# Optimization experiments

Measured on AMD Instinct MI355X. Metric: run time of the kernel, lower is better.

Reference implementation:

```python
import jax, jax.numpy as jnp
import numpy as np

HIDDEN = 4096
NUM_HEADS = 32
NUM_KV_HEADS = 8
HEAD_DIM = HIDDEN // NUM_HEADS  # 128
ROPE_THETA = 10000.0
T = 2048


def setup_inputs() -> dict:
    key = jax.random.key(0)
    k1, k2, k3 = jax.random.split(key, 3)
    positions = jnp.arange(T, dtype=jnp.int32)
    hidden_states = jax.random.normal(k1, (T, HIDDEN), dtype=jnp.float32)
    # 0.02 init scale keeps logits in a sane range
    Wqkv = jax.random.normal(k2, (HIDDEN, (NUM_HEADS + 2 * NUM_KV_HEADS) * HEAD_DIM), dtype=jnp.float32) * 0.02
    Wo = jax.random.normal(k3, (HIDDEN, HIDDEN), dtype=jnp.float32) * 0.02
    return {"positions": positions, "hidden_states": hidden_states, "Wqkv": Wqkv, "Wo": Wo}


def _rope_neox(x, positions):
    # x: [T, H, D]; neox style rotates halves of the head dim
    d2 = HEAD_DIM // 2
    inv_freq = ROPE_THETA ** (-jnp.arange(0, d2, dtype=jnp.float32) / d2)
    ang = positions.astype(jnp.float32)[:, None] * inv_freq  # [T, d2]
    cos = jnp.cos(ang)[:, None, :]  # [T,1,d2]
    sin = jnp.sin(ang)[:, None, :]
    x1, x2 = x[..., :d2], x[..., d2:]
    return jnp.concatenate([x1 * cos - x2 * sin, x2 * cos + x1 * sin], axis=-1)


def reference(positions, hidden_states, Wqkv, Wo):
    Tn = hidden_states.shape[0]
    q_sz = NUM_HEADS * HEAD_DIM
    kv_sz = NUM_KV_HEADS * HEAD_DIM
    qkv = hidden_states @ Wqkv  # [T, q_sz + 2*kv_sz]
    q = qkv[:, :q_sz].reshape(Tn, NUM_HEADS, HEAD_DIM)
    k = qkv[:, q_sz:q_sz + kv_sz].reshape(Tn, NUM_KV_HEADS, HEAD_DIM)
    v = qkv[:, q_sz + kv_sz:].reshape(Tn, NUM_KV_HEADS, HEAD_DIM)
    q = _rope_neox(q, positions)
    k = _rope_neox(k, positions)
    # GQA: repeat kv heads to match q heads
    rep = NUM_HEADS // NUM_KV_HEADS
    k = jnp.repeat(k, rep, axis=1)  # [T, H, D]
    v = jnp.repeat(v, rep, axis=1)
    scale = HEAD_DIM ** -0.5
    scores = jnp.einsum('thd,shd->hts', q, k) * scale  # [H, T, T]
    causal = positions[:, None] >= positions[None, :]  # [T, T]
    scores = jnp.where(causal[None, :, :], scores, jnp.float32(-1e30))
    probs = jax.nn.softmax(scores, axis=-1)
    attn = jnp.einsum('hts,shd->thd', probs, v).reshape(Tn, HIDDEN)
    return attn @ Wo
```

## Files before the change

### kernel.cpp

```cpp
#include <hip/hip_runtime.h>
#include <hip/hip_bf16.h>
#include <math.h>

#define T_SEQ 2048
#define HID   4096
#define NH    32
#define NKV   8
#define HD    128
#define QKVD  6144
#define KOFF  4096
#define VOFF  5120

typedef unsigned short u16;
typedef unsigned int   u32;
typedef __attribute__((ext_vector_type(4))) float f32x4;
typedef __attribute__((ext_vector_type(8))) short s16x8;
typedef __attribute__((ext_vector_type(4))) unsigned short u16x4;

__device__ inline u16 f2bf(float f) {
  u32 u = __float_as_uint(f);
  u32 r = u + 0x7FFFu + ((u >> 16) & 1u);
  return (u16)(r >> 16);
}
__device__ inline float bf2f(u16 h) { return __uint_as_float(((u32)h) << 16); }

__device__ inline void gl_lds16(const void* g, void* l) {
  __builtin_amdgcn_global_load_lds((const __attribute__((address_space(1))) void*)g,
                                   (__attribute__((address_space(3))) void*)l, 16, 0, 0);
}

__global__ void cast_f32_bf16(const float* __restrict__ in, u16* __restrict__ out, int n) {
  int i = (blockIdx.x * blockDim.x + threadIdx.x) * 4;
  if (i < n) {
    float4 v = *(const float4*)(in + i);
    u16x4 o = { f2bf(v.x), f2bf(v.y), f2bf(v.z), f2bf(v.w) };
    *(u16x4*)(out + i) = o;
  }
}

__global__ void transpose_cast(const float* __restrict__ in, u16* __restrict__ out, int K, int N) {
  __shared__ float tile[32][33];
  int n0 = blockIdx.x * 32, k0 = blockIdx.y * 32;
  int tx = threadIdx.x, ty = threadIdx.y;
  for (int i = ty; i < 32; i += 8)
    tile[i][tx] = in[(size_t)(k0 + i) * N + n0 + tx];
  __syncthreads();
  for (int i = ty; i < 32; i += 8)
    out[(size_t)(n0 + i) * K + k0 + tx] = f2bf(tile[tx][i]);
}

__global__ void vtrans(const u16* __restrict__ qkv, u16* __restrict__ Vt) {
  __shared__ u16 tile[32][33];
  int kv = blockIdx.z;
  int t0 = blockIdx.x * 32, d0 = blockIdx.y * 32;
  int tx = threadIdx.x, ty = threadIdx.y;
  for (int i = ty; i < 32; i += 8)
    tile[i][tx] = qkv[(size_t)(t0 + i) * QKVD + VOFF + kv * HD + d0 + tx];
  __syncthreads();
  for (int i = ty; i < 32; i += 8)
    Vt[(size_t)(kv * HD + d0 + i) * T_SEQ + t0 + tx] = tile[tx][i];
}

__global__ void rope_kernel(u16* __restrict__ qkv, const int* __restrict__ positions) {
  int t = blockIdx.x;
  int h = blockIdx.y * 4 + (threadIdx.x >> 6);
  int i = threadIdx.x & 63;
  float pos = (float)positions[t];
  float freq = exp2f(-(float)i * (13.287712379549449f / 64.0f));
  float ang = pos * freq;
  float s, c;
  sincosf(ang, &s, &c);
  size_t off;
  if (h < NH) off = (size_t)t * QKVD + h * HD;
  else        off = (size_t)t * QKVD + KOFF + (h - NH) * HD;
  float x1 = bf2f(qkv[off + i]);
  float x2 = bf2f(qkv[off + 64 + i]);
  qkv[off + i]      = f2bf(x1 * c - x2 * s);
  qkv[off + 64 + i] = f2bf(x2 * c + x1 * s);
}

__device__ inline void stage_half(const u16* __restrict__ G, int K, u16* lds, int w, int l) {
  const int rl = l >> 3;
  const int cs = ((l & 7) ^ rl) << 3;
#pragma unroll
  for (int i = 0; i < 2; i++) {
    const u16* src = G + (size_t)(8 * w + 64 * i + rl) * K + cs;
    gl_lds16(src, lds + (8 * w + 64 * i) * 64);
  }
}

#define LDA(i, kk) a[i][kk] = *(const s16x8*)(Ah + (((i) * 16 + lr) * 64) + ((((kk) * 4 + lg) ^ xsw) << 3))
#define LDB(j, kk) b[j][kk] = *(const s16x8*)(Bh + (((j) * 16 + lr) * 64) + ((((kk) * 4 + lg) ^ xsw) << 3))
#define MFMA_Q(i0, j0)                                                        \
  _Pragma("unroll") for (int i = 0; i < 4; i++)                               \
  _Pragma("unroll") for (int j = 0; j < 2; j++)                               \
  _Pragma("unroll") for (int kk = 0; kk < 2; kk++)                            \
    acc[i0 + i][j0 + j] = __builtin_amdgcn_mfma_f32_16x16x32_bf16(            \
        a[i0 + i][kk], b[j0 + j][kk], acc[i0 + i][j0 + j], 0, 0, 0);

template <bool BF16OUT>
__global__ __launch_bounds__(512, 2) void gemm256(const u16* __restrict__ A,
                                                  const u16* __restrict__ B,
                                                  void* __restrict__ Cv,
                                                  int M, int N, int K) {
  __shared__ __align__(16) u16 As[2][2][128 * 64];
  __shared__ __align__(16) u16 Bs[2][2][128 * 64];
  const int tid = threadIdx.x;
  const int w = tid >> 6, l = tid & 63;
  const int lr = l & 15, lg = l >> 4;
  const int wm = w >> 2, wn = w & 3;
  const int xsw = lr & 7;
  const int bm = blockIdx.y * 256, bn = blockIdx.x * 256;
  const int NT = K >> 6;

  const u16* Ab0 = A + (size_t)bm * K;
  const u16* Ab1 = A + (size_t)(bm + 128) * K;
  const u16* Bb0 = B + (size_t)bn * K;
  const u16* Bb1 = B + (size_t)(bn + 128) * K;

  f32x4 acc[8][4] = {};

  stage_half(Ab0, K, As[0][0], w, l);
  stage_half(Ab1, K, As[0][1], w, l);
  stage_half(Bb0, K, Bs[0][0], w, l);
  stage_half(Bb1, K, Bs[0][1], w, l);
  if (NT > 1) {
    stage_half(Ab0 + 64, K, As[1][0], w, l);
    stage_half(Ab1 + 64, K, As[1][1], w, l);
    asm volatile("s_waitcnt vmcnt(4)" ::: "memory");
  } else {
    asm volatile("s_waitcnt vmcnt(0)" ::: "memory");
  }
  __builtin_amdgcn_s_barrier();

  for (int t = 0; t < NT; t++) {
    const int cur = t & 1;
    const u16* Ah = &As[cur][wm][0];
    const u16* Bh = &Bs[cur][wn >> 1][(wn & 1) * 64 * 64];
    s16x8 a[8][2], b[4][2];

#pragma unroll
    for (int i = 0; i < 4; i++) { LDA(i, 0); LDA(i, 1); }
    LDB(0, 0); LDB(0, 1); LDB(1, 0); LDB(1, 1);
    if (t + 1 < NT) stage_half(Bb0 + (size_t)(t + 1) * 64, K, Bs[cur ^ 1][0], w, l);
    __builtin_amdgcn_s_barrier();
    asm volatile("s_waitcnt lgkmcnt(0)" ::: "memory");
    __builtin_amdgcn_s_setprio(1);
    MFMA_Q(0, 0)
    __builtin_amdgcn_s_setprio(0);
    __builtin_amdgcn_s_barrier();

#pragma unroll
    for (int i = 4; i < 8; i++) { LDA(i, 0); LDA(i, 1); }
    LDB(2, 0); LDB(2, 1); LDB(3, 0); LDB(3, 1);
    if (t + 1 < NT) stage_half(Bb1 + (size_t)(t + 1) * 64, K, Bs[cur ^ 1][1], w, l);
    __builtin_amdgcn_s_barrier();
    asm volatile("s_waitcnt lgkmcnt(0)" ::: "memory");
    __builtin_amdgcn_s_setprio(1);
    MFMA_Q(0, 2)
    __builtin_amdgcn_s_setprio(0);
    __builtin_amdgcn_s_barrier();

    if (t + 2 < NT) stage_half(Ab0 + (size_t)(t + 2) * 64, K, As[cur][0], w, l);
    __builtin_amdgcn_s_barrier();
    __builtin_amdgcn_s_setprio(1);
    MFMA_Q(4, 2)
    __builtin_amdgcn_s_setprio(0);
    __builtin_amdgcn_s_barrier();

    if (t + 2 < NT) {
      stage_half(Ab1 + (size_t)(t + 2) * 64, K, As[cur][1], w, l);
      asm volatile("s_waitcnt vmcnt(4)" ::: "memory");
    } else {
      asm volatile("s_waitcnt vmcnt(0)" ::: "memory");
    }
    __builtin_amdgcn_s_barrier();
    __builtin_amdgcn_s_setprio(1);
    MFMA_Q(4, 0)
    __builtin_amdgcn_s_setprio(0);
    __builtin_amdgcn_s_barrier();
  }

#pragma unroll
  for (int i = 0; i < 8; i++)
#pragma unroll
    for (int j = 0; j < 4; j++)
#pragma unroll
      for (int r = 0; r < 4; r++) {
        int row = bm + wm * 128 + i * 16 + lg * 4 + r;
        int col = bn + wn * 64 + j * 16 + lr;
        float v = acc[i][j][r];
        if (BF16OUT) ((u16*)Cv)[(size_t)row * N + col] = f2bf(v);
        else         ((float*)Cv)[(size_t)row * N + col] = v;
      }
}
#undef LDA
#undef LDB
#undef MFMA_Q

__device__ inline void stage_tiles(const u16* __restrict__ qkv, const u16* __restrict__ Vt,
                                   u16* Kb, u16* Vb, int kv0, int hkv, int w, int l) {
  const int krow_l = l >> 4;
  const int kcb = (l & 15) << 4;
  const int vrow_l = l >> 3;
  const int vcb = (l & 7) << 4;
#pragma unroll
  for (int c = 0; c < 4; c++) {
    int row = c * 16 + w * 4 + krow_l;
    const char* src = (const char*)(qkv + (size_t)(kv0 + row) * QKVD + KOFF + hkv * HD) +
                      (kcb ^ ((row & 7) << 4));
    gl_lds16(src, (char*)Kb + (c * 16 + w * 4) * 256);
  }
#pragma unroll
  for (int c = 0; c < 4; c++) {
    int row = c * 32 + w * 8 + vrow_l;
    const char* src = (const char*)(Vt + (size_t)(hkv * HD + row) * T_SEQ + kv0) +
                      (vcb ^ ((row & 7) << 4));
    gl_lds16(src, (char*)Vb + (c * 32 + w * 8) * 128);
  }
}

__global__ __launch_bounds__(256) void attn_fwd(const u16* __restrict__ qkv, const u16* __restrict__ Vt,
                                                u16* __restrict__ attnout) {
  __shared__ __align__(16) u16 Ks[2][64 * 128];
  __shared__ __align__(16) u16 Vs[2][128 * 64];
  __shared__ __align__(16) u16 plds[4][16 * 72];
  const int tid = threadIdx.x;
  const int w = tid >> 6, l = tid & 63;
  const int lr = l & 15, g = l >> 4;
  const int h = blockIdx.y;
  const int hkv = h >> 2;
  const int swzl = (lr & 7) << 4;
  const float scale = 0.08838834764831845f;
  u16* pw = &plds[w][0];

  for (int seg = 0; seg < 2; seg++) {
    const int qt = (seg == 0) ? blockIdx.x : (31 - blockIdx.x);
    const int q0 = qt * 64 + w * 16;
    const int q_abs = q0 + lr;

    s16x8 qf[4];
    const u16* qbase = qkv + (size_t)(q0 + lr) * QKVD + h * HD + g * 8;
#pragma unroll
    for (int kk = 0; kk < 4; kk++) qf[kk] = *(const s16x8*)(qbase + kk * 32);

    f32x4 acc_o[8] = {};
    float m_run = -__builtin_inff();
    float l_run = 0.0f;
    const int nt = qt + 1;

    stage_tiles(qkv, Vt, Ks[0], Vs[0], 0, hkv, w, l);
    asm volatile("s_waitcnt vmcnt(0)" ::: "memory");
    __syncthreads();
    int cur = 0;
    for (int kt = 0; kt < nt; kt++) {
      const int kv0 = kt * 64;
      if (kt + 1 < nt)
        stage_tiles(qkv, Vt, Ks[cur ^ 1], Vs[cur ^ 1], kv0 + 64, hkv, w, l);
      const bool masked = (kt == qt);

      f32x4 sa[4];
      const char* kb = (const char*)Ks[cur];
#pragma unroll
      for (int ct = 0; ct < 4; ct++) {
        f32x4 aa = {0.f, 0.f, 0.f, 0.f};
#pragma unroll
        for (int kk = 0; kk < 4; kk++) {
          s16x8 kf = *(const s16x8*)(kb + (ct * 16 + lr) * 256 + (((kk << 6) + (g << 4)) ^ swzl));
          aa = __builtin_amdgcn_mfma_f32_16x16x32_bf16(kf, qf[kk], aa, 0, 0, 0);
        }
        sa[ct] = aa;
      }

      float p[16];
      float pmax = -__builtin_inff();
#pragma unroll
      for (int ct = 0; ct < 4; ct++)
#pragma unroll
        for (int r = 0; r < 4; r++) {
          float s = sa[ct][r] * scale;
          if (masked) {
            int kv_abs = kv0 + ct * 16 + g * 4 + r;
            if (kv_abs > q_abs) s = -__builtin_inff();
          }
          p[ct * 4 + r] = s;
          pmax = fmaxf(pmax, s);
        }
      pmax = fmaxf(pmax, __shfl_xor(pmax, 16, 64));
      pmax = fmaxf(pmax, __shfl_xor(pmax, 32, 64));
      float m_new = fmaxf(m_run, pmax);
      float fac = __expf(m_run - m_new);
      float psum = 0.f;
#pragma unroll
      for (int x = 0; x < 16; x++) {
        float e = __expf(p[x] - m_new);
        p[x] = e;
        psum += e;
      }
      psum += __shfl_xor(psum, 16, 64);
      psum += __shfl_xor(psum, 32, 64);
      l_run = l_run * fac + psum;
      m_run = m_new;
      float fr[4];
#pragma unroll
      for (int r = 0; r < 4; r++) fr[r] = __shfl(fac, g * 4 + r, 64);
#pragma unroll
      for (int dt = 0; dt < 8; dt++)
#pragma unroll
        for (int r = 0; r < 4; r++) acc_o[dt][r] *= fr[r];

#pragma unroll
      for (int ct = 0; ct < 4; ct++) {
        u16x4 pk = { f2bf(p[ct * 4 + 0]), f2bf(p[ct * 4 + 1]), f2bf(p[ct * 4 + 2]), f2bf(p[ct * 4 + 3]) };
        *(u16x4*)(pw + lr * 72 + ct * 16 + g * 4) = pk;
      }
      asm volatile("s_waitcnt lgkmcnt(0)" ::: "memory");
      __builtin_amdgcn_sched_barrier(0);
      s16x8 pa0 = *(const s16x8*)(pw + lr * 72 + g * 8);
      s16x8 pa1 = *(const s16x8*)(pw + lr * 72 + 32 + g * 8);

      const char* vbb = (const char*)Vs[cur];
#pragma unroll
      for (int dt = 0; dt < 8; dt++) {
        s16x8 v0 = *(const s16x8*)(vbb + (dt * 16 + lr) * 128 + ((g << 4) ^ swzl));
        s16x8 v1 = *(const s16x8*)(vbb + (dt * 16 + lr) * 128 + ((64 + (g << 4)) ^ swzl));
        acc_o[dt] = __builtin_amdgcn_mfma_f32_16x16x32_bf16(pa0, v0, acc_o[dt], 0, 0, 0);
        acc_o[dt] = __builtin_amdgcn_mfma_f32_16x16x32_bf16(pa1, v1, acc_o[dt], 0, 0, 0);
      }
      asm volatile("s_waitcnt vmcnt(0)" ::: "memory");
      __syncthreads();
      cur ^= 1;
    }

    float ln[4];
#pragma unroll
    for (int r = 0; r < 4; r++) ln[r] = __shfl(l_run, g * 4 + r, 64);
#pragma unroll
    for (int dt = 0; dt < 8; dt++)
#pragma unroll
      for (int r = 0; r < 4; r++) {
        int row = q0 + g * 4 + r;
        int col = h * HD + dt * 16 + lr;
        attnout[(size_t)row * HID + col] = f2bf(acc_o[dt][r] / ln[r]);
      }
  }
}

extern "C" void kernel_launch(void* const* d_in, const int* in_sizes, int n_in,
                              void* d_out, int out_size, void* d_ws, size_t ws_size,
                              hipStream_t stream) {
  const int*   positions = (const int*)d_in[0];
  const float* X         = (const float*)d_in[1];
  const float* Wqkv      = (const float*)d_in[2];
  const float* Wo        = (const float*)d_in[3];
  float* out = (float*)d_out;

  char* ws = (char*)d_ws;
  size_t off = 0;
  u16* Xbf    = (u16*)(ws + off); off += (size_t)T_SEQ * HID * 2;
  u16* Wqkvt  = (u16*)(ws + off); off += (size_t)QKVD * HID * 2;
  u16* Wot    = (u16*)(ws + off); off += (size_t)HID * HID * 2;
  u16* qkv    = (u16*)(ws + off); off += (size_t)T_SEQ * QKVD * 2;
  u16* Vt     = (u16*)(ws + off); off += (size_t)NKV * HD * T_SEQ * 2;
  u16* attnb  = (u16*)(ws + off); off += (size_t)T_SEQ * HID * 2;

  cast_f32_bf16<<<dim3((T_SEQ * HID) / (256 * 4)), dim3(256), 0, stream>>>(X, Xbf, T_SEQ * HID);
  transpose_cast<<<dim3(QKVD / 32, HID / 32), dim3(32, 8), 0, stream>>>(Wqkv, Wqkvt, HID, QKVD);
  transpose_cast<<<dim3(HID / 32, HID / 32), dim3(32, 8), 0, stream>>>(Wo, Wot, HID, HID);
  gemm256<true><<<dim3(QKVD / 256, T_SEQ / 256), dim3(512), 0, stream>>>(Xbf, Wqkvt, qkv, T_SEQ, QKVD, HID);
  rope_kernel<<<dim3(T_SEQ, 10), dim3(256), 0, stream>>>(qkv, positions);
  vtrans<<<dim3(T_SEQ / 32, HD / 32, NKV), dim3(32, 8), 0, stream>>>(qkv, Vt);
  attn_fwd<<<dim3(16, 32), dim3(256), 0, stream>>>(qkv, Vt, attnb);
  gemm256<false><<<dim3(HID / 256, T_SEQ / 256), dim3(512), 0, stream>>>(attnb, Wot, out, T_SEQ, HID, HID);
}
```

Measured before the change: 585.7 us.

## Specialize QKV and output GEMMs with new tile shapes and triple buffering

Replaces the shared 256x256 GEMM with two specialized kernels. The QKV GEMM uses 256x192 tiles, giving 256 blocks instead of 192 to better fill the CUs. The output GEMM uses 128x256 tiles with a three-stage LDS ring buffer, giving 256 blocks and deeper prefetch. The goal is to reduce wave quantization and hide load latency, at the cost of lower per-block arithmetic intensity and more LDS per block.

```diff
diff --git a/kernel.cpp b/kernel.cpp
--- a/kernel.cpp
+++ b/kernel.cpp
@@ -79,104 +79,113 @@
   qkv[off + 64 + i] = f2bf(x2 * c + x1 * s);
 }
 
-__device__ inline void stage_half(const u16* __restrict__ G, int K, u16* lds, int w, int l) {
+__device__ inline void stage_unit(const u16* __restrict__ G, int K, u16* lds, int w, int l) {
   const int rl = l >> 3;
+  const int row = 8 * w + rl;
   const int cs = ((l & 7) ^ rl) << 3;
-#pragma unroll
-  for (int i = 0; i < 2; i++) {
-    const u16* src = G + (size_t)(8 * w + 64 * i + rl) * K + cs;
-    gl_lds16(src, lds + (8 * w + 64 * i) * 64);
-  }
-}
-
-#define LDA(i, kk) a[i][kk] = *(const s16x8*)(Ah + (((i) * 16 + lr) * 64) + ((((kk) * 4 + lg) ^ xsw) << 3))
-#define LDB(j, kk) b[j][kk] = *(const s16x8*)(Bh + (((j) * 16 + lr) * 64) + ((((kk) * 4 + lg) ^ xsw) << 3))
-#define MFMA_Q(i0, j0)                                                        \
-  _Pragma("unroll") for (int i = 0; i < 4; i++)                               \
-  _Pragma("unroll") for (int j = 0; j < 2; j++)                               \
-  _Pragma("unroll") for (int kk = 0; kk < 2; kk++)                            \
-    acc[i0 + i][j0 + j] = __builtin_amdgcn_mfma_f32_16x16x32_bf16(            \
-        a[i0 + i][kk], b[j0 + j][kk], acc[i0 + i][j0 + j], 0, 0, 0);
-
-template <bool BF16OUT>
-__global__ __launch_bounds__(512, 2) void gemm256(const u16* __restrict__ A,
-                                                  const u16* __restrict__ B,
-                                                  void* __restrict__ Cv,
-                                                  int M, int N, int K) {
-  __shared__ __align__(16) u16 As[2][2][128 * 64];
-  __shared__ __align__(16) u16 Bs[2][2][128 * 64];
+  gl_lds16(G + (size_t)row * K + cs, lds + 8 * w * 64);
+}
+
+#define RD(base, row) (*(const s16x8*)((base) + (size_t)(row) * 64 + ((((kk) * 4 + lg) ^ xsw) << 3)))
+#define MM(i, j) acc[i][j] = __builtin_amdgcn_mfma_f32_16x16x32_bf16(a[i][kk], b[j][kk], acc[i][j], 0, 0, 0)
+
+__global__ __launch_bounds__(512, 2) void gemm_qkv(const u16* __restrict__ A, const u16* __restrict__ B,
+                                                   u16* __restrict__ C, int M, int N, int K) {
+  __shared__ __align__(16) u16 As[2][256 * 64];
+  __shared__ __align__(16) u16 Bs[2][192 * 64];
   const int tid = threadIdx.x;
   const int w = tid >> 6, l = tid & 63;
   const int lr = l & 15, lg = l >> 4;
   const int wm = w >> 2, wn = w & 3;
   const int xsw = lr & 7;
-  const int bm = blockIdx.y * 256, bn = blockIdx.x * 256;
+  const int bm = blockIdx.y * 256, bn = blockIdx.x * 192;
   const int NT = K >> 6;
 
-  const u16* Ab0 = A + (size_t)bm * K;
-  const u16* Ab1 = A + (size_t)(bm + 128) * K;
-  const u16* Bb0 = B + (size_t)bn * K;
-  const u16* Bb1 = B + (size_t)(bn + 128) * K;
-
-  f32x4 acc[8][4] = {};
-
-  stage_half(Ab0, K, As[0][0], w, l);
-  stage_half(Ab1, K, As[0][1], w, l);
-  stage_half(Bb0, K, Bs[0][0], w, l);
-  stage_half(Bb1, K, Bs[0][1], w, l);
-  if (NT > 1) {
-    stage_half(Ab0 + 64, K, As[1][0], w, l);
-    stage_half(Ab1 + 64, K, As[1][1], w, l);
-    asm volatile("s_waitcnt vmcnt(4)" ::: "memory");
-  } else {
-    asm volatile("s_waitcnt vmcnt(0)" ::: "memory");
-  }
+  f32x4 acc[8][3] = {};
+  s16x8 a[8][2], b[3][2];
+
+#pragma unroll
+  for (int u = 0; u < 4; u++) stage_unit(A + (size_t)(bm + 64 * u) * K, K, As[0] + u * 4096, w, l);
+#pragma unroll
+  for (int u = 0; u < 3; u++) stage_unit(B + (size_t)(bn + 64 * u) * K, K, Bs[0] + u * 4096, w, l);
+#pragma unroll
+  for (int u = 0; u < 4; u++) stage_unit(A + (size_t)(bm + 64 * u) * K + 64, K, As[1] + u * 4096, w, l);
+  asm volatile("s_waitcnt vmcnt(4)" ::: "memory");
   __builtin_amdgcn_s_barrier();
 
   for (int t = 0; t < NT; t++) {
     const int cur = t & 1;
-    const u16* Ah = &As[cur][wm][0];
-    const u16* Bh = &Bs[cur][wn >> 1][(wn & 1) * 64 * 64];
-    s16x8 a[8][2], b[4][2];
-
-#pragma unroll
-    for (int i = 0; i < 4; i++) { LDA(i, 0); LDA(i, 1); }
-    LDB(0, 0); LDB(0, 1); LDB(1, 0); LDB(1, 1);
-    if (t + 1 < NT) stage_half(Bb0 + (size_t)(t + 1) * 64, K, Bs[cur ^ 1][0], w, l);
+    const u16* Ah = As[cur];
+    const u16* Bh = Bs[cur];
+    const int k1 = (t + 1) * 64, k2 = (t + 2) * 64;
+
+#pragma unroll
+    for (int kk = 0; kk < 2; kk++) {
+#pragma unroll
+      for (int i = 0; i < 4; i++) a[i][kk] = RD(Ah, wm * 128 + i * 16 + lr);
+#pragma unroll
+      for (int j = 0; j < 2; j++) b[j][kk] = RD(Bh, wn * 48 + j * 16 + lr);
+    }
+    if (t + 1 < NT) {
+      stage_unit(B + (size_t)(bn) * K + k1, K, Bs[cur ^ 1] + 0 * 4096, w, l);
+      stage_unit(B + (size_t)(bn + 64) * K + k1, K, Bs[cur ^ 1] + 1 * 4096, w, l);
+    }
     __builtin_amdgcn_s_barrier();
     asm volatile("s_waitcnt lgkmcnt(0)" ::: "memory");
-    __builtin_amdgcn_s_setprio(1);
-    MFMA_Q(0, 0)
-    __builtin_amdgcn_s_setprio(0);
-    __builtin_amdgcn_s_barrier();
-
-#pragma unroll
-    for (int i = 4; i < 8; i++) { LDA(i, 0); LDA(i, 1); }
-    LDB(2, 0); LDB(2, 1); LDB(3, 0); LDB(3, 1);
-    if (t + 1 < NT) stage_half(Bb1 + (size_t)(t + 1) * 64, K, Bs[cur ^ 1][1], w, l);
+    __builtin_amdgcn_sched_barrier(0);
+    __builtin_amdgcn_s_setprio(1);
+#pragma unroll
+    for (int kk = 0; kk < 2; kk++)
+#pragma unroll
+      for (int i = 0; i < 4; i++) { MM(i, 0); MM(i, 1); }
+    __builtin_amdgcn_s_setprio(0);
+    __builtin_amdgcn_s_barrier();
+
+#pragma unroll
+    for (int kk = 0; kk < 2; kk++) {
+#pragma unroll
+      for (int i = 4; i < 8; i++) a[i][kk] = RD(Ah, wm * 128 + i * 16 + lr);
+      b[2][kk] = RD(Bh, wn * 48 + 2 * 16 + lr);
+    }
+    if (t + 1 < NT)
+      stage_unit(B + (size_t)(bn + 128) * K + k1, K, Bs[cur ^ 1] + 2 * 4096, w, l);
     __builtin_amdgcn_s_barrier();
     asm volatile("s_waitcnt lgkmcnt(0)" ::: "memory");
-    __builtin_amdgcn_s_setprio(1);
-    MFMA_Q(0, 2)
-    __builtin_amdgcn_s_setprio(0);
-    __builtin_amdgcn_s_barrier();
-
-    if (t + 2 < NT) stage_half(Ab0 + (size_t)(t + 2) * 64, K, As[cur][0], w, l);
-    __builtin_amdgcn_s_barrier();
-    __builtin_amdgcn_s_setprio(1);
-    MFMA_Q(4, 2)
+    __builtin_amdgcn_sched_barrier(0);
+    __builtin_amdgcn_s_setprio(1);
+#pragma unroll
+    for (int kk = 0; kk < 2; kk++)
+#pragma unroll
+      for (int i = 0; i < 8; i++) MM(i, 2);
     __builtin_amdgcn_s_setprio(0);
     __builtin_amdgcn_s_barrier();
 
     if (t + 2 < NT) {
-      stage_half(Ab1 + (size_t)(t + 2) * 64, K, As[cur][1], w, l);
+      stage_unit(A + (size_t)(bm) * K + k2, K, As[cur] + 0 * 4096, w, l);
+      stage_unit(A + (size_t)(bm + 64) * K + k2, K, As[cur] + 1 * 4096, w, l);
+    }
+    __builtin_amdgcn_s_barrier();
+    __builtin_amdgcn_s_setprio(1);
+#pragma unroll
+    for (int kk = 0; kk < 2; kk++)
+#pragma unroll
+      for (int i = 4; i < 8; i++) MM(i, 0);
+    __builtin_amdgcn_s_setprio(0);
+    __builtin_amdgcn_s_barrier();
+
+    if (t + 2 < NT) {
+      stage_unit(A + (size_t)(bm + 128) * K + k2, K, As[cur] + 2 * 4096, w, l);
+      stage_unit(A + (size_t)(bm + 192) * K + k2, K, As[cur] + 3 * 4096, w, l);
       asm volatile("s_waitcnt vmcnt(4)" ::: "memory");
     } else {
       asm volatile("s_waitcnt vmcnt(0)" ::: "memory");
     }
     __builtin_amdgcn_s_barrier();
     __builtin_amdgcn_s_setprio(1);
-    MFMA_Q(4, 0)
+#pragma unroll
+    for (int kk = 0; kk < 2; kk++)
+#pragma unroll
+      for (int i = 4; i < 8; i++) MM(i, 1);
     __builtin_amdgcn_s_setprio(0);
     __builtin_amdgcn_s_barrier();
   }
@@ -184,19 +193,112 @@
 #pragma unroll
   for (int i = 0; i < 8; i++)
 #pragma unroll
-    for (int j = 0; j < 4; j++)
+    for (int j = 0; j < 3; j++)
 #pragma unroll
       for (int r = 0; r < 4; r++) {
         int row = bm + wm * 128 + i * 16 + lg * 4 + r;
+        int col = bn + wn * 48 + j * 16 + lr;
+        C[(size_t)row * N + col] = f2bf(acc[i][j][r]);
+      }
+}
+
+__global__ __launch_bounds__(512, 2) void gemm_out(const u16* __restrict__ A, const u16* __restrict__ B,
+                                                   float* __restrict__ C, int M, int N, int K) {
+  __shared__ __align__(16) u16 As3[3 * 128 * 64];
+  __shared__ __align__(16) u16 Bs3[3 * 256 * 64];
+  const int tid = threadIdx.x;
+  const int w = tid >> 6, l = tid & 63;
+  const int lr = l & 15, lg = l >> 4;
+  const int wm = w >> 2, wn = w & 3;
+  const int xsw = lr & 7;
+  const int bm = blockIdx.y * 128, bn = blockIdx.x * 256;
+  const int NT = K >> 6;
+
+  f32x4 acc[4][4] = {};
+  s16x8 a[4][2], b[4][2];
+
+#pragma unroll
+  for (int u = 0; u < 2; u++) stage_unit(A + (size_t)(bm + 64 * u) * K, K, As3 + u * 4096, w, l);
+#pragma unroll
+  for (int u = 0; u < 4; u++) stage_unit(B + (size_t)(bn + 64 * u) * K, K, Bs3 + u * 4096, w, l);
+#pragma unroll
+  for (int u = 0; u < 2; u++) stage_unit(A + (size_t)(bm + 64 * u) * K + 64, K, As3 + 8192 + u * 4096, w, l);
+#pragma unroll
+  for (int u = 0; u < 4; u++) stage_unit(B + (size_t)(bn + 64 * u) * K + 64, K, Bs3 + 16384 + u * 4096, w, l);
+  asm volatile("s_waitcnt vmcnt(6)" ::: "memory");
+  __builtin_amdgcn_s_barrier();
+
+  int cur = 0;
+  for (int t = 0; t < NT; t++) {
+    const u16* Ah = As3 + cur * 8192;
+    const u16* Bh = Bs3 + cur * 16384;
+    int sb = cur + 2; if (sb >= 3) sb -= 3;
+    u16* Asb = As3 + sb * 8192;
+    u16* Bsb = Bs3 + sb * 16384;
+    const int k2 = (t + 2) * 64;
+
+#pragma unroll
+    for (int kk = 0; kk < 2; kk++) {
+#pragma unroll
+      for (int i = 0; i < 4; i++) a[i][kk] = RD(Ah, wm * 64 + i * 16 + lr);
+#pragma unroll
+      for (int j = 0; j < 2; j++) b[j][kk] = RD(Bh, wn * 64 + j * 16 + lr);
+    }
+    if (t + 2 < NT) {
+      stage_unit(B + (size_t)(bn) * K + k2, K, Bsb + 0 * 4096, w, l);
+      stage_unit(B + (size_t)(bn + 64) * K + k2, K, Bsb + 1 * 4096, w, l);
+      stage_unit(B + (size_t)(bn + 128) * K + k2, K, Bsb + 2 * 4096, w, l);
+    }
+    __builtin_amdgcn_s_barrier();
+    asm volatile("s_waitcnt lgkmcnt(0)" ::: "memory");
+    __builtin_amdgcn_sched_barrier(0);
+    __builtin_amdgcn_s_setprio(1);
+#pragma unroll
+    for (int kk = 0; kk < 2; kk++)
+#pragma unroll
+      for (int i = 0; i < 4; i++) { MM(i, 0); MM(i, 1); }
+    __builtin_amdgcn_s_setprio(0);
+    __builtin_amdgcn_s_barrier();
+
+#pragma unroll
+    for (int kk = 0; kk < 2; kk++)
+#pragma unroll
+      for (int j = 2; j < 4; j++) b[j][kk] = RD(Bh, wn * 64 + j * 16 + lr);
+    if (t + 2 < NT) {
+      stage_unit(B + (size_t)(bn + 192) * K + k2, K, Bsb + 3 * 4096, w, l);
+      stage_unit(A + (size_t)(bm) * K + k2, K, Asb + 0 * 4096, w, l);
+      stage_unit(A + (size_t)(bm + 64) * K + k2, K, Asb + 1 * 4096, w, l);
+      asm volatile("s_waitcnt vmcnt(6)" ::: "memory");
+    } else {
+      asm volatile("s_waitcnt vmcnt(0)" ::: "memory");
+    }
+    __builtin_amdgcn_s_barrier();
+    asm volatile("s_waitcnt lgkmcnt(0)" ::: "memory");
+    __builtin_amdgcn_sched_barrier(0);
+    __builtin_amdgcn_s_setprio(1);
+#pragma unroll
+    for (int kk = 0; kk < 2; kk++)
+#pragma unroll
+      for (int i = 0; i < 4; i++) { MM(i, 2); MM(i, 3); }
+    __builtin_amdgcn_s_setprio(0);
+    __builtin_amdgcn_s_barrier();
+
+    cur = (cur == 2) ? 0 : cur + 1;
+  }
+
+#pragma unroll
+  for (int i = 0; i < 4; i++)
+#pragma unroll
+    for (int j = 0; j < 4; j++)
+#pragma unroll
+      for (int r = 0; r < 4; r++) {
+        int row = bm + wm * 64 + i * 16 + lg * 4 + r;
         int col = bn + wn * 64 + j * 16 + lr;
-        float v = acc[i][j][r];
-        if (BF16OUT) ((u16*)Cv)[(size_t)row * N + col] = f2bf(v);
-        else         ((float*)Cv)[(size_t)row * N + col] = v;
-      }
-}
-#undef LDA
-#undef LDB
-#undef MFMA_Q
+        C[(size_t)row * N + col] = acc[i][j][r];
+      }
+}
+#undef RD
+#undef MM
 
 __device__ inline void stage_tiles(const u16* __restrict__ qkv, const u16* __restrict__ Vt,
                                    u16* Kb, u16* Vb, int kv0, int hkv, int w, int l) {
@@ -367,9 +469,9 @@
   cast_f32_bf16<<<dim3((T_SEQ * HID) / (256 * 4)), dim3(256), 0, stream>>>(X, Xbf, T_SEQ * HID);
   transpose_cast<<<dim3(QKVD / 32, HID / 32), dim3(32, 8), 0, stream>>>(Wqkv, Wqkvt, HID, QKVD);
   transpose_cast<<<dim3(HID / 32, HID / 32), dim3(32, 8), 0, stream>>>(Wo, Wot, HID, HID);
-  gemm256<true><<<dim3(QKVD / 256, T_SEQ / 256), dim3(512), 0, stream>>>(Xbf, Wqkvt, qkv, T_SEQ, QKVD, HID);
+  gemm_qkv<<<dim3(QKVD / 192, T_SEQ / 256), dim3(512), 0, stream>>>(Xbf, Wqkvt, qkv, T_SEQ, QKVD, HID);
   rope_kernel<<<dim3(T_SEQ, 10), dim3(256), 0, stream>>>(qkv, positions);
   vtrans<<<dim3(T_SEQ / 32, HD / 32, NKV), dim3(32, 8), 0, stream>>>(qkv, Vt);
   attn_fwd<<<dim3(16, 32), dim3(256), 0, stream>>>(qkv, Vt, attnb);
-  gemm256<false><<<dim3(HID / 256, T_SEQ / 256), dim3(512), 0, stream>>>(attnb, Wot, out, T_SEQ, HID, HID);
-}
+  gemm_out<<<dim3(HID / 256, T_SEQ / 128), dim3(512), 0, stream>>>(attnb, Wot, out, T_SEQ, HID, HID);
+}
```

Measured after the change: 536.5 us. 1.09x faster.
